# Optimization experiments

Measured on AMD Instinct MI355X. Metric: run time of the kernel, lower is better.

## Reference

```python
import jax, jax.numpy as jnp
import numpy as np

B, N, D, H = 8, 1024, 512, 8
HEAD_DIM = D // H


def setup_inputs() -> dict:
    key = jax.random.key(0)
    k1, k2, k3, k4 = jax.random.split(key, 4)
    x = jax.random.normal(k1, (B, N, D), dtype=jnp.float32)
    relative_bias_logits = jax.random.normal(k2, (B, N, N, H), dtype=jnp.float32)
    # Dense params (fan-in scaled like lecun init)
    W_qkv = jax.random.normal(k3, (D, 3 * D), dtype=jnp.float32) / np.sqrt(D)
    b_qkv = jnp.zeros((3 * D,), dtype=jnp.float32)
    W_o = jax.random.normal(k4, (D, D), dtype=jnp.float32) / np.sqrt(D)
    b_o = jnp.zeros((D,), dtype=jnp.float32)
    return {"x": x, "relative_bias_logits": relative_bias_logits,
            "W_qkv": W_qkv, "b_qkv": b_qkv, "W_o": W_o, "b_o": b_o}


def reference(x, relative_bias_logits, W_qkv, b_qkv, W_o, b_o):
    # x: (B, N, D); relative_bias_logits: (B, N, N, H)
    n_heads = relative_bias_logits.shape[-1]
    emb = x.shape[-1]
    head_dim = emb // n_heads
    n = x.shape[-2]
    batch_dim = x.shape[:-2]

    qkv = x @ W_qkv + b_qkv                                   # (B, N, 3D)
    qkv = qkv.reshape(*batch_dim, n, n_heads, 3, head_dim)    # (B, N, H, 3, T)
    q, k, v = qkv[..., 0, :], qkv[..., 1, :], qkv[..., 2, :]  # each (B, N, H, T)

    logits = jnp.einsum('...QHT,...KHT->...QKH', q, k) / jnp.sqrt(
        jnp.asarray(head_dim, dtype=x.dtype))
    logits = logits + relative_bias_logits                    # (B, Q, K, H)
    # softmax over the K axis (axis=-2); jax.nn.softmax is max-stable
    attention = jax.nn.softmax(logits, axis=-2)
    # dropout deterministic (train=False): identity
    y = jnp.einsum('...QKH,...KHT->...QHT', attention, v)     # (B, N, H, T)
    y = y.reshape(*batch_dim, n, emb)                          # (B, N, D)
    y = y @ W_o + b_o
    return y
```

## Files before the change

kernel.cpp:

```cpp
#include <hip/hip_runtime.h>

typedef unsigned short u16;
typedef __attribute__((ext_vector_type(8))) short short8;
typedef __attribute__((ext_vector_type(4))) float f32x4;

__device__ __forceinline__ u16 f2bf(float f) {
  union { float f; unsigned u; } c; c.f = f;
  unsigned u = c.u;
  return (u16)((u + 0x7FFFu + ((u >> 16) & 1u)) >> 16);
}

__device__ __forceinline__ void gload16(const u16* g, u16* l) {
  __builtin_amdgcn_global_load_lds(
      (const __attribute__((address_space(1))) void*)g,
      (__attribute__((address_space(3))) void*)l, 16, 0, 0);
}

__global__ __launch_bounds__(256) void cvt_x_kernel(const float* __restrict__ x,
                                                    u16* __restrict__ xb) {
  int i = blockIdx.x * 256 + threadIdx.x;
  float4 v = ((const float4*)x)[i];
  uint2 st;
  st.x = (unsigned)f2bf(v.x) | ((unsigned)f2bf(v.y) << 16);
  st.y = (unsigned)f2bf(v.z) | ((unsigned)f2bf(v.w) << 16);
  ((uint2*)xb)[i] = st;
}

__global__ __launch_bounds__(256) void transp_kernel(const float* __restrict__ W,
                                                     u16* __restrict__ Wt, int NC) {
  __shared__ u16 tile[32][33];
  const int tx = threadIdx.x & 31, ty = threadIdx.x >> 5;
  const int n0 = blockIdx.x * 32, k0 = blockIdx.y * 32;
#pragma unroll
  for (int i = 0; i < 4; i++)
    tile[ty + i * 8][tx] = f2bf(W[(size_t)(k0 + ty + i * 8) * NC + n0 + tx]);
  __syncthreads();
#pragma unroll
  for (int i = 0; i < 4; i++)
    Wt[(size_t)(n0 + ty + i * 8) * 512 + k0 + tx] = tile[tx][ty + i * 8];
}

template<int MODE, int BN>
__global__ __launch_bounds__(256) void gemm_kernel(
    const u16* __restrict__ A, const u16* __restrict__ Bt,
    const float* __restrict__ biasv,
    u16* __restrict__ qb, u16* __restrict__ kb, u16* __restrict__ vtb,
    float* __restrict__ outp) {
  constexpr int BM = 128;
  constexpr int NI = BN / 32;
  __shared__ u16 As[BM * 64];
  __shared__ u16 Bs[BN * 64];
  const int tid = threadIdx.x;
  const int lane = tid & 63;
  const int w = tid >> 6, wm = w >> 1, wn = w & 1;
  const int m0 = blockIdx.y * BM, n0 = blockIdx.x * BN;
  const int lm = lane & 15, lg = lane >> 4;
  const int sr = tid >> 3, sc = (tid & 7) * 8;
  f32x4 acc[4][NI] = {};

  for (int k0 = 0; k0 < 512; k0 += 64) {
    __syncthreads();
#pragma unroll
    for (int c = 0; c < BM / 32; c++)
      gload16(&A[(size_t)(m0 + sr + c * 32) * 512 + k0 + sc], &As[c * 2048 + w * 512]);
#pragma unroll
    for (int c = 0; c < BN / 32; c++)
      gload16(&Bt[(size_t)(n0 + sr + c * 32) * 512 + k0 + sc], &Bs[c * 2048 + w * 512]);
    __syncthreads();
#pragma unroll
    for (int tc = 0; tc < 2; tc++) {
      short8 bf[NI];
#pragma unroll
      for (int ni = 0; ni < NI; ni++)
        bf[ni] = *(const short8*)&Bs[(wn * (BN / 2) + ni * 16 + lm) * 64 + tc * 32 + lg * 8];
#pragma unroll
      for (int mi = 0; mi < 4; mi++) {
        short8 af = *(const short8*)&As[(wm * 64 + mi * 16 + lm) * 64 + tc * 32 + lg * 8];
#pragma unroll
        for (int ni = 0; ni < NI; ni++)
          acc[mi][ni] = __builtin_amdgcn_mfma_f32_16x16x32_bf16(af, bf[ni], acc[mi][ni], 0, 0, 0);
      }
    }
  }

#pragma unroll
  for (int mi = 0; mi < 4; mi++)
#pragma unroll
    for (int ni = 0; ni < NI; ni++) {
      const int col = n0 + wn * (BN / 2) + ni * 16 + lm;
      const float bv = biasv[col];
#pragma unroll
      for (int r2 = 0; r2 < 4; r2++) {
        const int row = m0 + wm * 64 + mi * 16 + lg * 4 + r2;
        const float v = acc[mi][ni][r2] + bv;
        if (MODE == 0) {
          const int hh = col / 192, rem = col % 192;
          const int which = rem >> 6, t = rem & 63;
          const int b = row >> 10, n = row & 1023;
          const u16 bb = f2bf(v);
          if (which == 0)      qb[((size_t)(b * 8 + hh) * 1024 + n) * 64 + t] = bb;
          else if (which == 1) kb[((size_t)(b * 8 + hh) * 1024 + n) * 64 + t] = bb;
          else                 vtb[((size_t)(b * 8 + hh) * 64 + t) * 1024 + n] = bb;
        } else {
          outp[(size_t)row * 512 + col] = v;
        }
      }
    }
}

__global__ __launch_bounds__(512, 4) void attn_kernel(
    const u16* __restrict__ qb, const u16* __restrict__ kb,
    const u16* __restrict__ vtb, const float* __restrict__ bias,
    u16* __restrict__ yb) {
  __shared__ float biasS[2 * 8 * 16 * 34];
  __shared__ u16 Ps[8 * 16 * 40];
  const int tid = threadIdx.x;
  const int lane = tid & 63;
  const int h = tid >> 6;
  const int b = blockIdx.y;
  const int q0 = blockIdx.x * 16;
  const size_t bh = (size_t)b * 8 + h;
  const u16* Q  = qb  + bh * (1024 * 64);
  const u16* K  = kb  + bh * (1024 * 64);
  const u16* VT = vtb + bh * (64 * 1024);
  const int lm = lane & 15, lg = lane >> 4;

  short8 aq[2];
#pragma unroll
  for (int tc = 0; tc < 2; tc++)
    aq[tc] = *(const short8*)&Q[(size_t)(q0 + lm) * 64 + tc * 32 + lg * 8];

  f32x4 o[4] = {};
  float mrow[4], psum[4];
#pragma unroll
  for (int r2 = 0; r2 < 4; r2++) { mrow[r2] = -1e30f; psum[r2] = 0.f; }

  const float SC   = 0.125f * 1.4426950408889634f;
  const float LG2E = 1.4426950408889634f;

  const int kl = lane >> 1, h4 = (lane & 1) * 4;
  const size_t brow = (size_t)(b * 1024 + q0);

#pragma unroll
  for (int rr = 0; rr < 2; rr++) {
    const int qr = h + rr * 8;
    float4 p0 = *(const float4*)&bias[((brow + qr) * 1024 + kl) * 8 + h4];
    biasS[(h4 + 0) * 544 + qr * 34 + kl] = p0.x;
    biasS[(h4 + 1) * 544 + qr * 34 + kl] = p0.y;
    biasS[(h4 + 2) * 544 + qr * 34 + kl] = p0.z;
    biasS[(h4 + 3) * 544 + qr * 34 + kl] = p0.w;
  }
  __syncthreads();

  for (int it = 0; it < 32; it++) {
    const int kc = it * 32;
    const int bb = (it & 1) * 4352;

    float4 pre[2];
    const bool havePre = (it < 31);
    if (havePre) {
#pragma unroll
      for (int rr = 0; rr < 2; rr++) {
        const int qr = h + rr * 8;
        pre[rr] = *(const float4*)&bias[((brow + qr) * 1024 + kc + 32 + kl) * 8 + h4];
      }
    }

    f32x4 sf[2];
    __builtin_amdgcn_s_setprio(1);
#pragma unroll
    for (int kt = 0; kt < 2; kt++) {
      short8 bk0 = *(const short8*)&K[(size_t)(kc + kt * 16 + lm) * 64 + lg * 8];
      short8 bk1 = *(const short8*)&K[(size_t)(kc + kt * 16 + lm) * 64 + 32 + lg * 8];
      f32x4 c = {0.f, 0.f, 0.f, 0.f};
      c = __builtin_amdgcn_mfma_f32_16x16x32_bf16(aq[0], bk0, c, 0, 0, 0);
      c = __builtin_amdgcn_mfma_f32_16x16x32_bf16(aq[1], bk1, c, 0, 0, 0);
      sf[kt] = c;
    }
    __builtin_amdgcn_s_setprio(0);

    short8 bv[4];
#pragma unroll
    for (int nt = 0; nt < 4; nt++)
      bv[nt] = *(const short8*)&VT[(size_t)(nt * 16 + lm) * 1024 + kc + lg * 8];

    float pv2[2][4];
#pragma unroll
    for (int kt = 0; kt < 2; kt++)
#pragma unroll
      for (int r2 = 0; r2 < 4; r2++)
        pv2[kt][r2] = sf[kt][r2] * SC +
                      biasS[bb + h * 544 + (lg * 4 + r2) * 34 + kt * 16 + lm] * LG2E;
    float rmax[4];
#pragma unroll
    for (int r2 = 0; r2 < 4; r2++) rmax[r2] = fmaxf(pv2[0][r2], pv2[1][r2]);
#pragma unroll
    for (int d = 1; d < 16; d <<= 1)
#pragma unroll
      for (int r2 = 0; r2 < 4; r2++)
        rmax[r2] = fmaxf(rmax[r2], __shfl_xor(rmax[r2], d));
    const float g = fmaxf(fmaxf(rmax[0] - mrow[0], rmax[1] - mrow[1]),
                          fmaxf(rmax[2] - mrow[2], rmax[3] - mrow[3]));
    if (!__all(g <= 0.f)) {
#pragma unroll
      for (int r2 = 0; r2 < 4; r2++) {
        const float mn = fmaxf(mrow[r2], rmax[r2]);
        const float al = exp2f(mrow[r2] - mn);
        mrow[r2] = mn;
        psum[r2] *= al;
#pragma unroll
        for (int nt = 0; nt < 4; nt++) o[nt][r2] *= al;
      }
    }
#pragma unroll
    for (int kt = 0; kt < 2; kt++)
#pragma unroll
      for (int r2 = 0; r2 < 4; r2++) {
        const float p = exp2f(pv2[kt][r2] - mrow[r2]);
        psum[r2] += p;
        Ps[h * 640 + (lg * 4 + r2) * 40 + kt * 16 + lm] = f2bf(p);
      }

    short8 ap = *(const short8*)&Ps[h * 640 + lm * 40 + lg * 8];
    __builtin_amdgcn_s_setprio(1);
#pragma unroll
    for (int nt = 0; nt < 4; nt++)
      o[nt] = __builtin_amdgcn_mfma_f32_16x16x32_bf16(ap, bv[nt], o[nt], 0, 0, 0);
    __builtin_amdgcn_s_setprio(0);

    if (havePre) {
      const int nb = ((it + 1) & 1) * 4352;
#pragma unroll
      for (int rr = 0; rr < 2; rr++) {
        const int qr = h + rr * 8;
        biasS[nb + (h4 + 0) * 544 + qr * 34 + kl] = pre[rr].x;
        biasS[nb + (h4 + 1) * 544 + qr * 34 + kl] = pre[rr].y;
        biasS[nb + (h4 + 2) * 544 + qr * 34 + kl] = pre[rr].z;
        biasS[nb + (h4 + 3) * 544 + qr * 34 + kl] = pre[rr].w;
      }
      __syncthreads();
    }
  }

  float lr[4];
#pragma unroll
  for (int r2 = 0; r2 < 4; r2++) {
    float s = psum[r2];
#pragma unroll
    for (int d = 1; d < 16; d <<= 1) s += __shfl_xor(s, d);
    lr[r2] = s;
  }
#pragma unroll
  for (int nt = 0; nt < 4; nt++)
#pragma unroll
    for (int r2 = 0; r2 < 4; r2++) {
      const int row = q0 + lg * 4 + r2;
      yb[((size_t)(b * 1024 + row)) * 512 + h * 64 + nt * 16 + lm] = f2bf(o[nt][r2] / lr[r2]);
    }
}

extern "C" void kernel_launch(void* const* d_in, const int* in_sizes, int n_in,
                              void* d_out, int out_size, void* d_ws, size_t ws_size,
                              hipStream_t stream) {
  const float* x    = (const float*)d_in[0];
  const float* bias = (const float*)d_in[1];
  const float* Wqkv = (const float*)d_in[2];
  const float* bqkv = (const float*)d_in[3];
  const float* Wo   = (const float*)d_in[4];
  const float* bo   = (const float*)d_in[5];
  float* out = (float*)d_out;

  char* p = (char*)d_ws;
  u16* xb    = (u16*)p; p += (size_t)8192 * 512 * 2;
  u16* wqkvT = (u16*)p; p += (size_t)1536 * 512 * 2;
  u16* woT   = (u16*)p; p += (size_t)512 * 512 * 2;
  u16* qB    = (u16*)p; p += (size_t)8 * 8 * 1024 * 64 * 2;
  u16* kB    = (u16*)p; p += (size_t)8 * 8 * 1024 * 64 * 2;
  u16* vtB   = (u16*)p; p += (size_t)8 * 8 * 64 * 1024 * 2;
  u16* yB    = (u16*)p; p += (size_t)8192 * 512 * 2;

  cvt_x_kernel<<<4096, 256, 0, stream>>>(x, xb);
  transp_kernel<<<dim3(48, 16), 256, 0, stream>>>(Wqkv, wqkvT, 1536);
  transp_kernel<<<dim3(16, 16), 256, 0, stream>>>(Wo, woT, 512);
  gemm_kernel<0, 128><<<dim3(12, 64), 256, 0, stream>>>(xb, wqkvT, bqkv, qB, kB, vtB, nullptr);
  attn_kernel<<<dim3(64, 8), 512, 0, stream>>>(qB, kB, vtB, bias, yB);
  gemm_kernel<1, 64><<<dim3(8, 64), 256, 0, stream>>>(yB, woT, bo, nullptr, nullptr, nullptr, out);
}
```

Before: 531.8 us.

## Deepen bias prefetch to two chunks ahead and remap blocks across batches

The attention kernel's bias streaming is restructured into a two-iteration unrolled loop that keeps two register buffers of bias loads in flight, issuing the global load two chunks ahead instead of one. The loads become nontemporal, and the barrier is a raw s_barrier after waiting only on LDS counters. Block indices are also remapped so consecutive blocks cover different batches. The goal is to hide the latency of the large, HBM-bound bias read, at the cost of more registers and a hand-written barrier that relies on correct waitcnt semantics.

```diff
diff --git a/kernel.cpp b/kernel.cpp
--- a/kernel.cpp
+++ b/kernel.cpp
@@ -112,13 +112,14 @@
     const u16* __restrict__ qb, const u16* __restrict__ kb,
     const u16* __restrict__ vtb, const float* __restrict__ bias,
     u16* __restrict__ yb) {
-  __shared__ float biasS[2 * 8 * 16 * 34];
+  __shared__ float biasS[2 * 4352];
   __shared__ u16 Ps[8 * 16 * 40];
   const int tid = threadIdx.x;
   const int lane = tid & 63;
   const int h = tid >> 6;
-  const int b = blockIdx.y;
-  const int q0 = blockIdx.x * 16;
+  const int linear = blockIdx.x + (blockIdx.y << 6);
+  const int b = linear & 7;
+  const int q0 = (linear >> 3) * 16;
   const size_t bh = (size_t)b * 8 + h;
   const u16* Q  = qb  + bh * (1024 * 64);
   const u16* K  = kb  + bh * (1024 * 64);
@@ -141,30 +142,33 @@
   const int kl = lane >> 1, h4 = (lane & 1) * 4;
   const size_t brow = (size_t)(b * 1024 + q0);
 
-#pragma unroll
-  for (int rr = 0; rr < 2; rr++) {
-    const int qr = h + rr * 8;
-    float4 p0 = *(const float4*)&bias[((brow + qr) * 1024 + kl) * 8 + h4];
-    biasS[(h4 + 0) * 544 + qr * 34 + kl] = p0.x;
-    biasS[(h4 + 1) * 544 + qr * 34 + kl] = p0.y;
-    biasS[(h4 + 2) * 544 + qr * 34 + kl] = p0.z;
-    biasS[(h4 + 3) * 544 + qr * 34 + kl] = p0.w;
-  }
-  __syncthreads();
-
-  for (int it = 0; it < 32; it++) {
+  auto loadPre = [&](int chunk, f32x4* pre) {
+#pragma unroll
+    for (int rr = 0; rr < 2; rr++) {
+      const int qr = h + rr * 8;
+      pre[rr] = __builtin_nontemporal_load(
+          (const f32x4*)&bias[((brow + qr) * 1024 + chunk * 32 + kl) * 8 + h4]);
+    }
+  };
+  auto writePre = [&](const f32x4* pre, int nb) {
+#pragma unroll
+    for (int rr = 0; rr < 2; rr++) {
+      const int qr = h + rr * 8;
+      biasS[nb + (h4 + 0) * 544 + qr * 34 + kl] = pre[rr][0];
+      biasS[nb + (h4 + 1) * 544 + qr * 34 + kl] = pre[rr][1];
+      biasS[nb + (h4 + 2) * 544 + qr * 34 + kl] = pre[rr][2];
+      biasS[nb + (h4 + 3) * 544 + qr * 34 + kl] = pre[rr][3];
+    }
+  };
+  auto barrier = [&]() {
+    asm volatile("s_waitcnt lgkmcnt(0)" ::: "memory");
+    __builtin_amdgcn_s_barrier();
+    __builtin_amdgcn_sched_barrier(0);
+  };
+
+  auto compute = [&](int it) {
     const int kc = it * 32;
-    const int bb = (it & 1) * 4352;
-
-    float4 pre[2];
-    const bool havePre = (it < 31);
-    if (havePre) {
-#pragma unroll
-      for (int rr = 0; rr < 2; rr++) {
-        const int qr = h + rr * 8;
-        pre[rr] = *(const float4*)&bias[((brow + qr) * 1024 + kc + 32 + kl) * 8 + h4];
-      }
-    }
+    const int bbS = (it & 1) * 4352;
 
     f32x4 sf[2];
     __builtin_amdgcn_s_setprio(1);
@@ -190,7 +194,7 @@
 #pragma unroll
       for (int r2 = 0; r2 < 4; r2++)
         pv2[kt][r2] = sf[kt][r2] * SC +
-                      biasS[bb + h * 544 + (lg * 4 + r2) * 34 + kt * 16 + lm] * LG2E;
+                      biasS[bbS + h * 544 + (lg * 4 + r2) * 34 + kt * 16 + lm] * LG2E;
     float rmax[4];
 #pragma unroll
     for (int r2 = 0; r2 < 4; r2++) rmax[r2] = fmaxf(pv2[0][r2], pv2[1][r2]);
@@ -227,18 +231,26 @@
     for (int nt = 0; nt < 4; nt++)
       o[nt] = __builtin_amdgcn_mfma_f32_16x16x32_bf16(ap, bv[nt], o[nt], 0, 0, 0);
     __builtin_amdgcn_s_setprio(0);
-
-    if (havePre) {
-      const int nb = ((it + 1) & 1) * 4352;
-#pragma unroll
-      for (int rr = 0; rr < 2; rr++) {
-        const int qr = h + rr * 8;
-        biasS[nb + (h4 + 0) * 544 + qr * 34 + kl] = pre[rr].x;
-        biasS[nb + (h4 + 1) * 544 + qr * 34 + kl] = pre[rr].y;
-        biasS[nb + (h4 + 2) * 544 + qr * 34 + kl] = pre[rr].z;
-        biasS[nb + (h4 + 3) * 544 + qr * 34 + kl] = pre[rr].w;
-      }
-      __syncthreads();
+  };
+
+  f32x4 preA[2], preB[2];
+  loadPre(0, preA);
+  writePre(preA, 0);
+  loadPre(1, preA);
+  barrier();
+
+#pragma unroll 1
+  for (int it2 = 0; it2 < 16; it2++) {
+    const int i0 = it2 * 2, i1 = i0 + 1;
+    if (i0 + 2 < 32) loadPre(i0 + 2, preB);
+    compute(i0);
+    writePre(preA, ((i0 + 1) & 1) * 4352);
+    barrier();
+    if (i1 + 2 < 32) loadPre(i1 + 2, preA);
+    compute(i1);
+    if (i1 < 31) {
+      writePre(preB, ((i1 + 1) & 1) * 4352);
+      barrier();
     }
   }
 
```

Result: faster. 512.4 us (-3.6%).
